# Kernel optimization log

Hardware: AMD Instinct MI355X
Metric: run time of the kernel (lower is better)

Reference implementation:

```python
import jax, jax.numpy as jnp
import numpy as np


def setup_inputs() -> dict:
    key = jax.random.key(0)
    k1, k2, k3 = jax.random.split(key, 3)
    B, S_enc, S_dec, D = 8, 4096, 4096, 128
    b = jax.random.normal(k1, (B, S_enc, D), dtype=jnp.float32)
    h = jax.random.normal(k2, (B, S_dec, D), dtype=jnp.float32)
    W_b = jax.random.normal(k3, (D, D), dtype=jnp.float32) * (1.0 / np.sqrt(D))
    return {"b": b, "h": h, "W_b": W_b}


def reference(b, h, W_b):
    # tmp1 = h @ W_b : [B, S_dec, D]
    tmp1 = jnp.einsum('btd,de->bte', h, W_b)
    # scores = tmp1 @ b^T : [B, S_dec, S_enc]
    scores = jnp.einsum('bte,bse->bts', tmp1, b)
    attn = jax.nn.softmax(scores, axis=-1)
    # weighted sum over encoder positions (the original does this via a huge
    # tile/broadcast/multiply/reduce_sum; math is a batched matmul)
    cxt = jnp.einsum('bts,bsd->btd', attn, b)
    return cxt
```

## Files before the change

kernel.cpp:

```cpp
#include <hip/hip_runtime.h>

typedef _Float16 half2v __attribute__((ext_vector_type(2)));
typedef _Float16 half4 __attribute__((ext_vector_type(4)));
typedef _Float16 half8 __attribute__((ext_vector_type(8)));
typedef float floatx4 __attribute__((ext_vector_type(4)));

#define B_   8
#define SE   4096
#define SD   4096
#define D_   128
#define NT   64
#define LDB  136
#define LOG2E 1.44269504f

__device__ __forceinline__ void cp16_async(const _Float16* g, _Float16* l) {
    __builtin_amdgcn_global_load_lds((const __attribute__((address_space(1))) unsigned int*)g,
                                     (__attribute__((address_space(3))) unsigned int*)l, 16, 0, 0);
}

__device__ __forceinline__ float dot2acc(half2v a, half2v b, float c) {
#if __has_builtin(__builtin_amdgcn_fdot2)
    return __builtin_amdgcn_fdot2(a, b, c, false);
#else
    return c + (float)a[0] * (float)b[0] + (float)a[1] * (float)b[1];
#endif
}

__global__ __launch_bounds__(512) void bprep(const float* __restrict__ b,
                                             const float* __restrict__ W,
                                             _Float16* __restrict__ kc,
                                             _Float16* __restrict__ vT,
                                             _Float16* __restrict__ Wt16,
                                             _Float16* __restrict__ Wtlo) {
    __shared__ _Float16 bs[64 * 128];
    const int bb = blockIdx.y, s0 = blockIdx.x * 64;
    const int tid = threadIdx.x;

    if (blockIdx.x == 0) {
        int base = bb * 2048 + tid * 4;
        #pragma unroll
        for (int j = 0; j < 4; ++j) {
            int i = base + j;
            int d = i >> 7, e = i & 127;
            float w = W[i];
            _Float16 hi = (_Float16)w;
            Wt16[e * 128 + d] = hi;
            Wtlo[e * 128 + d] = (_Float16)(w - (float)hi);
        }
    }

    const float* bg = b + ((size_t)bb * SE + s0) * D_;
    _Float16* kg = kc + ((size_t)bb * SE + s0) * D_;
    #pragma unroll
    for (int it = 0; it < 2; ++it) {
        int idx = tid + it * 512;
        int row = idx >> 4, seg = idx & 15;
        const float* src = bg + row * D_ + seg * 8;
        float4 a = *(const float4*)src;
        float4 c = *(const float4*)(src + 4);
        half8 hv;
        hv[0] = (_Float16)a.x; hv[1] = (_Float16)a.y; hv[2] = (_Float16)a.z; hv[3] = (_Float16)a.w;
        hv[4] = (_Float16)c.x; hv[5] = (_Float16)c.y; hv[6] = (_Float16)c.z; hv[7] = (_Float16)c.w;
        *(half8*)(kg + row * D_ + seg * 8) = hv;
        *(half8*)(bs + row * 128 + ((seg ^ (row & 15)) * 8)) = hv;
    }
    __syncthreads();

    const int sg = tid & 15, dg = tid >> 4;
    half4 rowv[4];
    #pragma unroll
    for (int j = 0; j < 4; ++j) {
        int r = sg * 4 + j;
        rowv[j] = *(const half4*)(bs + r * 128 + (((dg >> 1) ^ (r & 15)) * 8) + (dg & 1) * 4);
    }
    #pragma unroll
    for (int dd = 0; dd < 4; ++dd) {
        half4 o;
        #pragma unroll
        for (int j = 0; j < 4; ++j) o[j] = rowv[j][dd];
        *(half4*)(vT + ((size_t)bb * D_ + dg * 4 + dd) * SE + s0 + sg * 4) = o;
    }
}

__global__ __launch_bounds__(512, 4) void flash(const float* __restrict__ h,
                                                const _Float16* __restrict__ Wt16,
                                                const _Float16* __restrict__ Wtlo,
                                                const _Float16* __restrict__ kc,
                                                const _Float16* __restrict__ vT,
                                                float* __restrict__ out) {
    __shared__ _Float16 KV[2][16384];

    const int lin = blockIdx.y * 64 + blockIdx.x;
    const int swz = ((lin & 7) << 6) + (lin >> 3);
    const int bb  = swz >> 6;
    const int q0  = (swz & 63) * 64;

    const int tid  = threadIdx.x;
    const int wave = tid >> 6;
    const int wq   = wave >> 1;
    const int ws   = wave & 1;
    const int lane = tid & 63;
    const int l15  = lane & 15;
    const int quad = lane >> 4;

    const _Float16* kbase = kc + (size_t)bb * SE * D_;
    const _Float16* vbase = vT + (size_t)bb * D_ * SE;

    int koff[2], voff[2];
    #pragma unroll
    for (int it = 0; it < 2; ++it) {
        int i = it * 512 + wave * 64 + lane;
        int kr = i >> 4, kpp = i & 15;
        int km = kr & 15;
        int srow = (kr & 32) + ((km >> 2) << 3) + (((kr >> 4) & 1) << 2) + (km & 3);
        koff[it] = srow * D_ + ((kpp ^ km) * 8);
        int vr = i >> 3, vpp = i & 7;
        voff[it] = vr * SE + ((vpp ^ (vr & 7)) * 8);
    }

    const _Float16* kA0[4]; const _Float16* kA1[4];
    const _Float16 *vB0, *vB1;
    #pragma unroll
    for (int ks = 0; ks < 4; ++ks) {
        int o = l15 * 128 + (((ks * 4 + quad) ^ l15) * 8) + ws * 4096;
        kA0[ks] = &KV[0][o]; kA1[ks] = &KV[1][o];
    }
    {
        int o = 8192 + l15 * 64 + (((ws * 4 + quad) ^ (l15 & 7)) * 8);
        vB0 = &KV[0][o]; vB1 = &KV[1][o];
    }

    {
        _Float16* buf0 = &KV[0][0];
        #pragma unroll
        for (int it = 0; it < 2; ++it) {
            cp16_async(kbase + koff[it], buf0 + (it * 512 + wave * 64) * 8);
            cp16_async(vbase + voff[it], buf0 + 8192 + (it * 512 + wave * 64) * 8);
        }
    }

    _Float16* hs = &KV[1][0];
    {
        const float* hg = h + ((size_t)bb * SD + q0) * D_;
        #pragma unroll
        for (int it = 0; it < 2; ++it) {
            int idx = tid + it * 512;
            int row = idx >> 4, seg = idx & 15;
            const float* src = hg + row * D_ + seg * 8;
            float4 a = *(const float4*)src;
            float4 c = *(const float4*)(src + 4);
            half8 hv;
            hv[0] = (_Float16)a.x; hv[1] = (_Float16)a.y; hv[2] = (_Float16)a.z; hv[3] = (_Float16)a.w;
            hv[4] = (_Float16)c.x; hv[5] = (_Float16)c.y; hv[6] = (_Float16)c.z; hv[7] = (_Float16)c.w;
            *(half8*)(hs + row * LDB + seg * 8) = hv;
        }
    }
    __syncthreads();
    half8 qf[4];
    {
        half8 af[4];
        #pragma unroll
        for (int ks = 0; ks < 4; ++ks)
            af[ks] = *(const half8*)(hs + (wq * 16 + l15) * LDB + ks * 32 + quad * 8);
        floatx4 acc[4];
        #pragma unroll
        for (int nt = 0; nt < 4; ++nt) acc[nt] = (floatx4){0.f, 0.f, 0.f, 0.f};
        #pragma unroll
        for (int ks = 0; ks < 4; ++ks) {
            #pragma unroll
            for (int nt = 0; nt < 4; ++nt) {
                size_t wo = (size_t)(ws * 64 + nt * 16 + l15) * 128 + ks * 32 + quad * 8;
                half8 bh = *(const half8*)(Wt16 + wo);
                half8 bl = *(const half8*)(Wtlo + wo);
                acc[nt] = __builtin_amdgcn_mfma_f32_16x16x32_f16(af[ks], bh, acc[nt], 0, 0, 0);
                acc[nt] = __builtin_amdgcn_mfma_f32_16x16x32_f16(af[ks], bl, acc[nt], 0, 0, 0);
            }
        }
        __syncthreads();
        #pragma unroll
        for (int nt = 0; nt < 4; ++nt)
            #pragma unroll
            for (int r = 0; r < 4; ++r)
                hs[(wq * 16 + quad * 4 + r) * LDB + ws * 64 + nt * 16 + l15] =
                    (_Float16)(acc[nt][r] * LOG2E);
        __syncthreads();
        #pragma unroll
        for (int ks = 0; ks < 4; ++ks)
            qf[ks] = *(const half8*)(hs + (wq * 16 + l15) * LDB + ks * 32 + quad * 8);
    }

    floatx4 acc_o[8];
    #pragma unroll
    for (int dt = 0; dt < 8; ++dt) acc_o[dt] = (floatx4){0.f, 0.f, 0.f, 0.f};
    float nm = 0.f;
    float l_part = 0.f;
    const half2v one2 = { (_Float16)1.f, (_Float16)1.f };

#define STEP(T, KA, VBP, NBUF)                                                        \
  {                                                                                   \
    __syncthreads();                  \
    if ((T) + 1 < SE / NT) {                                                          \
      const _Float16* kt = kbase + (size_t)((T) + 1) * (NT * D_);                     \
      const _Float16* vt = vbase + (size_t)((T) + 1) * NT;                            \
      _Float16* bufn = (NBUF);                                                        \
      _Pragma("unroll")                                                               \
      for (int it = 0; it < 2; ++it) {                                                \
        cp16_async(kt + koff[it], bufn + (it * 512 + wave * 64) * 8);                 \
        cp16_async(vt + voff[it], bufn + 8192 + (it * 512 + wave * 64) * 8);          \
      }                                                                               \
    }                                                                                 \
                        \
    floatx4 accs[2];                                                                  \
    accs[0] = (floatx4){nm, nm, nm, nm};                                              \
    accs[1] = accs[0];                                                                \
    __builtin_amdgcn_s_setprio(1);                                                    \
    _Pragma("unroll")                                                                 \
    for (int ks = 0; ks < 4; ++ks) {                                                  \
      half8 af0 = *(const half8*)(KA[ks]);                                            \
      half8 af1 = *(const half8*)(KA[ks] + 2048);                                     \
      accs[0] = __builtin_amdgcn_mfma_f32_16x16x32_f16(af0, qf[ks], accs[0], 0, 0, 0);\
      accs[1] = __builtin_amdgcn_mfma_f32_16x16x32_f16(af1, qf[ks], accs[1], 0, 0, 0);\
    }                                                                                 \
    __builtin_amdgcn_s_setprio(0);                                                    \
       \
    half8 vf[8];                                                                      \
    _Pragma("unroll")                                                                 \
    for (int dt = 0; dt < 8; ++dt)                                                    \
      vf[dt] = *(const half8*)((VBP) + dt * 1024);                                    \
                                     \
    float x0 = fmaxf(fmaxf(accs[0][0], accs[0][1]), accs[0][2]);                      \
    float x1 = fmaxf(fmaxf(accs[0][3], accs[1][0]), accs[1][1]);                      \
    float x2 = fmaxf(fmaxf(accs[1][2], accs[1][3]), x0);                              \
    float mv = fmaxf(x1, x2);                                                         \
    if (__ballot(mv > 11.5f) != 0ull) {              \
      float mr = fmaxf(mv, __shfl_xor(mv, 16, 64));                                   \
      mr = fmaxf(mr, __shfl_xor(mr, 32, 64));                                         \
      float delta = fmaxf(mr, 0.f);                                                   \
      float alpha = exp2f(-delta);                                                    \
      l_part *= alpha;                                                                \
      float ab[4];                                                                    \
      _Pragma("unroll")                                                               \
      for (int r = 0; r < 4; ++r) ab[r] = __shfl(alpha, quad * 4 + r, 64);            \
      _Pragma("unroll")                                                               \
      for (int dt = 0; dt < 8; ++dt)                                                  \
        _Pragma("unroll")                                                             \
        for (int r = 0; r < 4; ++r) acc_o[dt][r] *= ab[r];                            \
      _Pragma("unroll")                                                               \
      for (int stl = 0; stl < 2; ++stl)                                               \
        _Pragma("unroll")                                                             \
        for (int r = 0; r < 4; ++r) accs[stl][r] -= delta;                            \
      nm -= delta;                                                                    \
    }                                                                                 \
         \
    float p0 = exp2f(accs[0][0]), p1 = exp2f(accs[0][1]);                             \
    float p2 = exp2f(accs[0][2]), p3 = exp2f(accs[0][3]);                             \
    float p4 = exp2f(accs[1][0]), p5 = exp2f(accs[1][1]);                             \
    float p6 = exp2f(accs[1][2]), p7 = exp2f(accs[1][3]);                             \
    half2v c0 = __builtin_bit_cast(half2v, __builtin_amdgcn_cvt_pkrtz(p0, p1));       \
    half2v c1 = __builtin_bit_cast(half2v, __builtin_amdgcn_cvt_pkrtz(p2, p3));       \
    half2v c2 = __builtin_bit_cast(half2v, __builtin_amdgcn_cvt_pkrtz(p4, p5));       \
    half2v c3 = __builtin_bit_cast(half2v, __builtin_amdgcn_cvt_pkrtz(p6, p7));       \
    l_part = dot2acc(c0, one2, l_part);                                               \
    l_part = dot2acc(c1, one2, l_part);                                               \
    l_part = dot2acc(c2, one2, l_part);                                               \
    l_part = dot2acc(c3, one2, l_part);                                               \
    half8 pA;                                                                         \
    pA[0] = c0[0]; pA[1] = c0[1]; pA[2] = c1[0]; pA[3] = c1[1];                       \
    pA[4] = c2[0]; pA[5] = c2[1]; pA[6] = c3[0]; pA[7] = c3[1];                       \
       \
    __builtin_amdgcn_s_setprio(1);                                                    \
    _Pragma("unroll")                                                                 \
    for (int dt = 0; dt < 8; ++dt)                                                    \
      acc_o[dt] = __builtin_amdgcn_mfma_f32_16x16x32_f16(pA, vf[dt], acc_o[dt], 0, 0, 0); \
    __builtin_amdgcn_s_setprio(0);                                                    \
  }

    for (int t = 0; t < SE / NT; t += 2) {
        STEP(t,     kA0, vB0, &KV[1][0]);
        STEP(t + 1, kA1, vB1, &KV[0][0]);
    }
#undef STEP

    const float m_q = -nm;
    float l_own;
    {
        float l = l_part;
        l += __shfl_xor(l, 16, 64);
        l += __shfl_xor(l, 32, 64);
        l_own = l;
    }

    __syncthreads();
    float* Ob = (float*)&KV[0][0];
    float* ml = (float*)&KV[1][0];

    if (ws == 1) {
        #pragma unroll
        for (int dt = 0; dt < 8; ++dt)
            *(floatx4*)(Ob + ((wq * 8 + dt) * 64 + lane) * 4) = acc_o[dt];
        if (quad == 0)
            *(float2*)(ml + (wq * 16 + l15) * 2) = make_float2(m_q, l_own);
    }
    __syncthreads();
    if (ws == 0) {
        float m0r[4], l0r[4], m1r[4], l1r[4];
        #pragma unroll
        for (int r = 0; r < 4; ++r) {
            m0r[r] = __shfl(m_q, quad * 4 + r, 64);
            l0r[r] = __shfl(l_own, quad * 4 + r, 64);
            float2 p = *(float2*)(ml + (wq * 16 + quad * 4 + r) * 2);
            m1r[r] = p.x; l1r[r] = p.y;
        }
        float a0[4], a1[4], inv[4];
        #pragma unroll
        for (int r = 0; r < 4; ++r) {
            float mm = fmaxf(m0r[r], m1r[r]);
            a0[r] = exp2f(m0r[r] - mm);
            a1[r] = exp2f(m1r[r] - mm);
            inv[r] = 1.f / (l0r[r] * a0[r] + l1r[r] * a1[r]);
        }
        float* orow = out + ((size_t)bb * SD + q0 + wq * 16 + quad * 4) * D_;
        #pragma unroll
        for (int dt = 0; dt < 8; ++dt) {
            floatx4 o1 = *(floatx4*)(Ob + ((wq * 8 + dt) * 64 + lane) * 4);
            #pragma unroll
            for (int r = 0; r < 4; ++r)
                orow[(size_t)r * D_ + dt * 16 + l15] =
                    (acc_o[dt][r] * a0[r] + o1[r] * a1[r]) * inv[r];
        }
    }
}

extern "C" void kernel_launch(void* const* d_in, const int* in_sizes, int n_in,
                              void* d_out, int out_size, void* d_ws, size_t ws_size,
                              hipStream_t stream) {
    const float* b = (const float*)d_in[0];
    const float* h = (const float*)d_in[1];
    const float* W = (const float*)d_in[2];
    float* out = (float*)d_out;

    _Float16* Wt16 = (_Float16*)d_ws;
    _Float16* Wtlo = Wt16 + 128 * 128;
    _Float16* kc   = Wtlo + 128 * 128;
    _Float16* vT   = kc + (size_t)B_ * SE * D_;

    bprep<<<dim3(SE / 64, B_), 512, 0, stream>>>(b, W, kc, vT, Wt16, Wtlo);
    flash<<<dim3(SD / 64, B_), 512, 0, stream>>>(h, Wt16, Wtlo, kc, vT, out);
}
```

Measured before the change: 186.9 us.

## Software-pipeline attention loop so next tile's QK overlaps current softmax and PV

The monolithic per-tile STEP macro is split into PREFETCH, QKSTEP, VREAD, SMAX and PVSTEP pieces, and the loop is reordered with a prologue and epilogue. Each iteration now computes the QK scores for the next K tile right after the barrier, before running the PV MFMAs for the current tile. Independent MFMA work can then interleave with the exp2 and max reductions of the online softmax. The cost is longer live ranges for accs, vf and pA, which adds register pressure, plus more complex barrier and buffer ordering that must keep the double-buffer hazards correct.

Result: slower. 393.7 us (+110.6%).

```diff
diff --git a/kernel.cpp b/kernel.cpp
--- a/kernel.cpp
+++ b/kernel.cpp
@@ -196,21 +196,23 @@
     float l_part = 0.f;
     const half2v one2 = { (_Float16)1.f, (_Float16)1.f };
 
-#define STEP(T, KA, VBP, NBUF)                                                        \
-  {                                                                                   \
-    __syncthreads();                  \
-    if ((T) + 1 < SE / NT) {                                                          \
-      const _Float16* kt = kbase + (size_t)((T) + 1) * (NT * D_);                     \
-      const _Float16* vt = vbase + (size_t)((T) + 1) * NT;                            \
+    floatx4 accs[2];
+    half8 vf[8];
+    half8 pA;
+
+#define PREFETCH(T2, NBUF)                                                            \
+    {                                                                                 \
+      const _Float16* kt = kbase + (size_t)(T2) * (NT * D_);                          \
+      const _Float16* vt = vbase + (size_t)(T2) * NT;                                 \
       _Float16* bufn = (NBUF);                                                        \
       _Pragma("unroll")                                                               \
       for (int it = 0; it < 2; ++it) {                                                \
         cp16_async(kt + koff[it], bufn + (it * 512 + wave * 64) * 8);                 \
         cp16_async(vt + voff[it], bufn + 8192 + (it * 512 + wave * 64) * 8);          \
       }                                                                               \
-    }                                                                                 \
-                        \
-    floatx4 accs[2];                                                                  \
+    }
+
+#define QKSTEP(KA)                                                                    \
     accs[0] = (floatx4){nm, nm, nm, nm};                                              \
     accs[1] = accs[0];                                                                \
     __builtin_amdgcn_s_setprio(1);                                                    \
@@ -221,14 +223,14 @@
       accs[0] = __builtin_amdgcn_mfma_f32_16x16x32_f16(af0, qf[ks], accs[0], 0, 0, 0);\
       accs[1] = __builtin_amdgcn_mfma_f32_16x16x32_f16(af1, qf[ks], accs[1], 0, 0, 0);\
     }                                                                                 \
-    __builtin_amdgcn_s_setprio(0);                                                    \
-       \
-    half8 vf[8];                                                                      \
+    __builtin_amdgcn_s_setprio(0);
+
+#define VREAD(VBP)                                                                    \
     _Pragma("unroll")                                                                 \
-    for (int dt = 0; dt < 8; ++dt)                                                    \
-      vf[dt] = *(const half8*)((VBP) + dt * 1024);                                    \
-                                     \
-    float x0 = fmaxf(fmaxf(accs[0][0], accs[0][1]), accs[0][2]);                      \
+    for (int dt = 0; dt < 8; ++dt) vf[dt] = *(const half8*)((VBP) + dt * 1024);
+
+#define SMAX()                                                                        \
+  { float x0 = fmaxf(fmaxf(accs[0][0], accs[0][1]), accs[0][2]);                      \
     float x1 = fmaxf(fmaxf(accs[0][3], accs[1][0]), accs[1][1]);                      \
     float x2 = fmaxf(fmaxf(accs[1][2], accs[1][3]), x0);                              \
     float mv = fmaxf(x1, x2);                                                         \
@@ -251,7 +253,6 @@
         for (int r = 0; r < 4; ++r) accs[stl][r] -= delta;                            \
       nm -= delta;                                                                    \
     }                                                                                 \
-         \
     float p0 = exp2f(accs[0][0]), p1 = exp2f(accs[0][1]);                             \
     float p2 = exp2f(accs[0][2]), p3 = exp2f(accs[0][3]);                             \
     float p4 = exp2f(accs[1][0]), p5 = exp2f(accs[1][1]);                             \
@@ -264,22 +265,48 @@
     l_part = dot2acc(c1, one2, l_part);                                               \
     l_part = dot2acc(c2, one2, l_part);                                               \
     l_part = dot2acc(c3, one2, l_part);                                               \
-    half8 pA;                                                                         \
     pA[0] = c0[0]; pA[1] = c0[1]; pA[2] = c1[0]; pA[3] = c1[1];                       \
-    pA[4] = c2[0]; pA[5] = c2[1]; pA[6] = c3[0]; pA[7] = c3[1];                       \
-       \
+    pA[4] = c2[0]; pA[5] = c2[1]; pA[6] = c3[0]; pA[7] = c3[1]; }
+
+#define PVSTEP()                                                                      \
     __builtin_amdgcn_s_setprio(1);                                                    \
     _Pragma("unroll")                                                                 \
     for (int dt = 0; dt < 8; ++dt)                                                    \
       acc_o[dt] = __builtin_amdgcn_mfma_f32_16x16x32_f16(pA, vf[dt], acc_o[dt], 0, 0, 0); \
-    __builtin_amdgcn_s_setprio(0);                                                    \
-  }
-
-    for (int t = 0; t < SE / NT; t += 2) {
-        STEP(t,     kA0, vB0, &KV[1][0]);
-        STEP(t + 1, kA1, vB1, &KV[0][0]);
-    }
-#undef STEP
+    __builtin_amdgcn_s_setprio(0);
+
+    __syncthreads();
+    PREFETCH(1, &KV[1][0]);
+    QKSTEP(kA0);
+
+    for (int t = 0; t < SE / NT - 2; t += 2) {
+        VREAD(vB0);
+        SMAX();
+        __syncthreads();
+        PREFETCH(t + 2, &KV[0][0]);
+        QKSTEP(kA1);
+        PVSTEP();
+        VREAD(vB1);
+        SMAX();
+        __syncthreads();
+        PREFETCH(t + 3, &KV[1][0]);
+        QKSTEP(kA0);
+        PVSTEP();
+    }
+    VREAD(vB0);
+    SMAX();
+    __syncthreads();
+    QKSTEP(kA1);
+    PVSTEP();
+    VREAD(vB1);
+    SMAX();
+    PVSTEP();
+
+#undef PREFETCH
+#undef QKSTEP
+#undef VREAD
+#undef SMAX
+#undef PVSTEP
 
     const float m_q = -nm;
     float l_own;
```
